# Kernel optimization log

Hardware: AMD Instinct MI355X
Metric: run time of the kernel (lower is better)

Reference implementation:

```python
import jax, jax.numpy as jnp
import numpy as np


def pixel_coordinates(h, w):
    # (h, w, 2) grid of (x, y) in [-1, 1]
    y = jnp.linspace(-1.0, 1.0, h)
    x = jnp.linspace(-1.0, 1.0, w)
    yy, xx = jnp.meshgrid(y, x, indexing='ij')
    return jnp.stack([xx, yy], axis=-1)


def base_grid(h_in, w_in):
    y = jnp.linspace(-1.0 + 1.0 / h_in, 1.0 - 1.0 / h_in, h_in)
    x = jnp.linspace(-1.0 + 1.0 / w_in, 1.0 - 1.0 / w_in, w_in)
    yy, xx = jnp.meshgrid(y, x, indexing='ij')
    return jnp.stack([xx, yy], axis=-1)  # [h_in, w_in, 2]


def setup_inputs() -> dict:
    key = jax.random.key(0)
    params = jax.random.normal(key, (2, 9, 32, 32), dtype=jnp.float32)
    return {"params": params, "h_out": 128, "w_out": 128}


def reference(params, h_out, w_out):
    B, _, h_in, w_in = params.shape
    N = h_in * w_in
    p = jnp.transpose(params, (0, 2, 3, 1))  # [B, h_in, w_in, 9]

    # positions (mu): base grid + tanh(offset) * (2/h_in)
    mu = base_grid(h_in, w_in)[None] + jnp.tanh(p[..., 0:2]) * (2.0 / h_in)
    mu = mu.reshape(B, N, 2)

    # covariance via Cholesky-like factor L = [[exp(a), 0], [b, exp(c)]]
    v1x = jnp.exp(p[..., 2])
    v2x = p[..., 3]
    v2y = jnp.exp(p[..., 4])
    zero = jnp.zeros_like(v1x)
    L = jnp.stack([jnp.stack([v1x, zero], axis=-1),
                   jnp.stack([v2x, v2y], axis=-1)], axis=-2)  # [B,h,w,2,2]
    cov = L @ jnp.swapaxes(L, -1, -2)
    cov = cov.reshape(B, N, 2, 2) + jnp.eye(2, dtype=params.dtype) * 1e-5
    Sigma_inv = jnp.linalg.inv(cov)  # [B, N, 2, 2]

    colors = jax.nn.sigmoid(p[..., 5:8]).reshape(B, N, 3)
    opacities = jax.nn.sigmoid(p[..., 8]).reshape(B, N)

    coords = pixel_coordinates(h_out, w_out)  # [H, W, 2]
    dx = coords[None, None] - mu[:, :, None, None, :]  # [B, N, H, W, 2]
    exponent = -0.5 * jnp.einsum('bnhwi,bnij,bnhwj->bnhw', dx, Sigma_inv, dx)
    exponent = jnp.clip(exponent, -20.0, 20.0)
    kernel = jnp.exp(exponent)  # [B, N, H, W]

    weights = opacities[:, :, None, None] * kernel
    weights_sum = jnp.sum(weights, axis=1, keepdims=True) + 1e-8
    norm_w = weights / weights_sum  # [B, N, H, W]
    image = jnp.einsum('bnhw,bnc->bchw', norm_w, colors)  # [B, 3, H, W]
    return image
```

## Files before the change

kernel.cpp:

```cpp
#include <hip/hip_runtime.h>


#define NB   2
#define NG   1024
#define HOUT 128
#define WOUT 128
#define NPW  16

typedef float v2f __attribute__((ext_vector_type(2)));

__device__ __forceinline__ float fast_exp(float x) {
    return __builtin_amdgcn_exp2f(x * 1.4426950408889634f);
}
__device__ __forceinline__ float fast_sigmoid(float x) {
    float e = __builtin_amdgcn_exp2f(-x * 1.4426950408889634f);
    return __builtin_amdgcn_rcpf(1.0f + e);
}
__device__ __forceinline__ float fast_tanh(float x) {
    float e = __builtin_amdgcn_exp2f(-x * 2.8853900817779268f);
    return fmaf(2.0f, __builtin_amdgcn_rcpf(1.0f + e), -1.0f);
}

template<int CTRL, int RM>
__device__ __forceinline__ float dpp_add(float v) {
    int s = __builtin_amdgcn_update_dpp(0, __float_as_int(v), CTRL, RM, 0xF, true);
    return v + __int_as_float(s);
}
__device__ __forceinline__ float wave_sum(float v) {
    v = dpp_add<0x111, 0xF>(v);
    v = dpp_add<0x112, 0xF>(v);
    v = dpp_add<0x114, 0xF>(v);
    v = dpp_add<0x118, 0xF>(v);
    v = dpp_add<0x142, 0xA>(v);
    v = dpp_add<0x143, 0xC>(v);
    return v;
}

struct Coefs { float A, B2, C; };
__device__ __forceinline__ Coefs cov_coefs(float p2, float p3, float p4) {
    float ea  = fast_exp(p2);
    float ec  = fast_exp(p4);
    float c00 = ea * ea + 1e-5f;
    float c01 = p3 * ea;
    float c11 = p3 * p3 + ec * ec + 1e-5f;
    float det = c00 * c11 - c01 * c01;
    float id  = 1.0f / det;
    const float s = -0.72134752044448169f;
    Coefs r;
    r.A  = s * c11 * id;
    r.B2 = -2.0f * s * c01 * id;
    r.C  = s * c00 * id;
    return r;
}

__global__ __launch_bounds__(256, 2) void gauss_all(const float* __restrict__ params,
                                                    float* __restrict__ out) {
    const int tid  = threadIdx.x;
    const int lane = tid & 63;
    const int wv   = tid >> 6;
    const int blk  = blockIdx.x;
    const int b    = blk >> 8;
    const int pix0 = (((blk & 255) << 2) + wv) * NPW;

    v2f rec[8][9];
    const float* P = params + b * 9 * NG;
    #pragma unroll
    for (int k = 0; k < 8; ++k) {
        const int n0 = 2 * lane + 128 * k;
        v2f p[9];
        #pragma unroll
        for (int f = 0; f < 9; ++f)
            p[f] = *(const v2f*)(P + f * NG + n0);

        const float gw = (float)(n0 & 31);
        const float gh = (float)(n0 >> 5);
        v2f mux2, muy2, A2, B22, C2;
        mux2.x = -0.96875f + gw * 0.0625f + fast_tanh(p[0].x) * 0.0625f;
        mux2.y = -0.96875f + (gw + 1.0f) * 0.0625f + fast_tanh(p[0].y) * 0.0625f;
        muy2.x = -0.96875f + gh * 0.0625f + fast_tanh(p[1].x) * 0.0625f;
        muy2.y = -0.96875f + gh * 0.0625f + fast_tanh(p[1].y) * 0.0625f;
        Coefs cx = cov_coefs(p[2].x, p[3].x, p[4].x);
        Coefs cy = cov_coefs(p[2].y, p[3].y, p[4].y);
        A2.x = cx.A; B22.x = cx.B2; C2.x = cx.C;
        A2.y = cy.A; B22.y = cy.B2; C2.y = cy.C;
        v2f op2, ocr2, ocg2, ocb2;
        op2.x  = fast_sigmoid(p[8].x);         op2.y  = fast_sigmoid(p[8].y);
        ocr2.x = op2.x * fast_sigmoid(p[5].x); ocr2.y = op2.y * fast_sigmoid(p[5].y);
        ocg2.x = op2.x * fast_sigmoid(p[6].x); ocg2.y = op2.y * fast_sigmoid(p[6].y);
        ocb2.x = op2.x * fast_sigmoid(p[7].x); ocb2.y = op2.y * fast_sigmoid(p[7].y);

        rec[k][0] = mux2; rec[k][1] = muy2; rec[k][2] = A2;
        rec[k][3] = B22;  rec[k][4] = C2;   rec[k][5] = op2;
        rec[k][6] = ocr2; rec[k][7] = ocg2; rec[k][8] = ocb2;
    }

    const int w0 = pix0 & 127;
    const int h0 = pix0 >> 7;
    const float py = -1.0f + (float)h0 * (2.0f / 127.0f);
    const v2f py2 = {py, py};
    float* ob = out + b * 3 * (HOUT * WOUT) + pix0;

    #pragma unroll 2
    for (int i = 0; i < NPW; ++i) {
        const float px = -1.0f + (float)(w0 + i) * (2.0f / 127.0f);
        const v2f px2 = {px, px};
        v2f wsum2 = {0.0f, 0.0f}, ar2 = {0.0f, 0.0f};
        v2f ag2   = {0.0f, 0.0f}, ab2 = {0.0f, 0.0f};

        #pragma unroll
        for (int k = 0; k < 8; ++k) {
            v2f dx = px2 - rec[k][0];
            v2f dy = py2 - rec[k][1];
            v2f m  = rec[k][2] * dx;
            m      = __builtin_elementwise_fma(rec[k][3], dy, m);
            v2f t  = rec[k][4] * dy;
            v2f e2 = __builtin_elementwise_fma(t, dy, m * dx);
            e2 = __builtin_elementwise_max(e2, (v2f){-28.853900817779268f,
                                                     -28.853900817779268f});
            v2f k2 = {__builtin_amdgcn_exp2f(e2.x), __builtin_amdgcn_exp2f(e2.y)};
            wsum2 = __builtin_elementwise_fma(rec[k][5], k2, wsum2);
            ar2   = __builtin_elementwise_fma(rec[k][6], k2, ar2);
            ag2   = __builtin_elementwise_fma(rec[k][7], k2, ag2);
            ab2   = __builtin_elementwise_fma(rec[k][8], k2, ab2);
        }

        float ws = wave_sum(wsum2.x + wsum2.y);
        float rr = wave_sum(ar2.x + ar2.y);
        float gg = wave_sum(ag2.x + ag2.y);
        float bb = wave_sum(ab2.x + ab2.y);

        if (lane == 63) {
            float inv = 1.0f / (ws + 1e-8f);
            ob[i]                   = rr * inv;
            ob[i + HOUT * WOUT]     = gg * inv;
            ob[i + 2 * HOUT * WOUT] = bb * inv;
        }
    }
}

extern "C" void kernel_launch(void* const* d_in, const int* in_sizes, int n_in,
                              void* d_out, int out_size, void* d_ws, size_t ws_size,
                              hipStream_t stream) {
    const float* params = (const float*)d_in[0];
    float* out = (float*)d_out;
    (void)d_ws; (void)ws_size;

    hipLaunchKernelGGL(gauss_all, dim3(512), dim3(256), 0, stream, params, out);
}
```

Measured before the change: 72.81 us.

## Split gaussian set across wave pairs and combine partial sums in LDS

Each pixel strip is now handled by two waves, each covering half of the 1024 gaussians, so per-thread precomputed records shrink from 8 to 4 pairs and the grid doubles to 1024 blocks. Partial weight and color sums are written to shared memory, and after a block barrier 32 threads combine the pairs, normalise and store coalesced outputs. This is meant to halve register pressure and raise parallelism and occupancy on the many CUs. In exchange every gaussian's parameters are recomputed twice as often across blocks, and a barrier plus an LDS round trip is added.

Result: slower. 74.32 us (+2.1%).

```diff
diff --git a/kernel.cpp b/kernel.cpp
--- a/kernel.cpp
+++ b/kernel.cpp
@@ -53,20 +53,25 @@
     return r;
 }
 
-__global__ __launch_bounds__(256, 2) void gauss_all(const float* __restrict__ params,
-                                                    float* __restrict__ out) {
+__global__ __launch_bounds__(256, 2) void gauss_half(const float* __restrict__ params,
+                                                     float* __restrict__ out) {
+    __shared__ float4 sred[4][NPW];
+
     const int tid  = threadIdx.x;
     const int lane = tid & 63;
     const int wv   = tid >> 6;
+    const int ps   = wv >> 1;
+    const int half = wv & 1;
     const int blk  = blockIdx.x;
-    const int b    = blk >> 8;
-    const int pix0 = (((blk & 255) << 2) + wv) * NPW;
+    const int b    = blk >> 9;
+    const int pixb = ((blk & 511) << 5);
+    const int pix0 = pixb + ps * NPW;
 
-    v2f rec[8][9];
+    v2f rec[4][9];
     const float* P = params + b * 9 * NG;
     #pragma unroll
-    for (int k = 0; k < 8; ++k) {
-        const int n0 = 2 * lane + 128 * k;
+    for (int k = 0; k < 4; ++k) {
+        const int n0 = half * 512 + 2 * lane + 128 * k;
         v2f p[9];
         #pragma unroll
         for (int f = 0; f < 9; ++f)
@@ -98,7 +103,6 @@
     const int h0 = pix0 >> 7;
     const float py = -1.0f + (float)h0 * (2.0f / 127.0f);
     const v2f py2 = {py, py};
-    float* ob = out + b * 3 * (HOUT * WOUT) + pix0;
 
     #pragma unroll 2
     for (int i = 0; i < NPW; ++i) {
@@ -108,7 +112,7 @@
         v2f ag2   = {0.0f, 0.0f}, ab2 = {0.0f, 0.0f};
 
         #pragma unroll
-        for (int k = 0; k < 8; ++k) {
+        for (int k = 0; k < 4; ++k) {
             v2f dx = px2 - rec[k][0];
             v2f dy = py2 - rec[k][1];
             v2f m  = rec[k][2] * dx;
@@ -128,13 +132,22 @@
         float rr = wave_sum(ar2.x + ar2.y);
         float gg = wave_sum(ag2.x + ag2.y);
         float bb = wave_sum(ab2.x + ab2.y);
+        if (lane == 63) sred[wv][i] = make_float4(ws, rr, gg, bb);
+    }
+    __syncthreads();
 
-        if (lane == 63) {
-            float inv = 1.0f / (ws + 1e-8f);
-            ob[i]                   = rr * inv;
-            ob[i + HOUT * WOUT]     = gg * inv;
-            ob[i + 2 * HOUT * WOUT] = bb * inv;
-        }
+    if (tid < 32) {
+        const int cps = tid >> 4;
+        const int i   = tid & 15;
+        float4 a = sred[cps * 2][i];
+        float4 c = sred[cps * 2 + 1][i];
+        float ws = a.x + c.x, rr = a.y + c.y, gg = a.z + c.z, bb = a.w + c.w;
+        float inv = 1.0f / (ws + 1e-8f);
+        const int pix = pixb + cps * NPW + i;
+        float* ob = out + b * 3 * (HOUT * WOUT) + pix;
+        ob[0]               = rr * inv;
+        ob[HOUT * WOUT]     = gg * inv;
+        ob[2 * HOUT * WOUT] = bb * inv;
     }
 }
 
@@ -145,5 +158,5 @@
     float* out = (float*)d_out;
     (void)d_ws; (void)ws_size;
 
-    hipLaunchKernelGGL(gauss_all, dim3(512), dim3(256), 0, stream, params, out);
+    hipLaunchKernelGGL(gauss_half, dim3(1024), dim3(256), 0, stream, params, out);
 }
```
